# Optimization experiments

Hardware: AMD Instinct MI355X
Metric: run time of the kernel (lower is better)

Reference implementation:

```python
import jax, jax.numpy as jnp
import numpy as np

N, E = 50000, 800000
IN_FEATS, H, F = 128, 2, 64
NEG_SLOPE = 0.2


def _gat_conv(x, W, attn_l, attn_r, bias, src, dst):
    """DGL-style GATConv. x:[N,IN], W:[H*F,IN], attn_l/attn_r:[H,F], bias:[H*F]. Returns [N,H,F]."""
    z = (x @ W.T).reshape(N, H, F)                      # node projections
    el = jnp.einsum('nhf,hf->nh', z, attn_l)            # [N,H]
    er = jnp.einsum('nhf,hf->nh', z, attn_r)            # [N,H]
    e = jax.nn.leaky_relu(el[src] + er[dst], NEG_SLOPE) # [E,H] edge logits
    # edge softmax over incoming edges of each destination node
    m = jax.ops.segment_max(e, dst, num_segments=N)     # [N,H]
    ex = jnp.exp(e - m[dst])
    s = jax.ops.segment_sum(ex, dst, num_segments=N)    # [N,H]
    alpha = ex / s[dst]                                 # [E,H]
    msg = alpha[:, :, None] * z[src]                    # [E,H,F]
    out = jax.ops.segment_sum(msg, dst, num_segments=N) # [N,H,F]
    return out + bias.reshape(1, H, F)


def setup_inputs() -> dict:
    key = jax.random.key(0)
    ks = jax.random.split(key, 10)
    x = jax.random.normal(ks[0], (N, IN_FEATS), dtype=jnp.float32)
    h = jax.random.normal(ks[1], (N, H, F), dtype=jnp.float32)
    src = jax.random.randint(ks[2], (E,), 0, N, dtype=jnp.int32)
    dst = jax.random.randint(ks[3], (E,), 0, N, dtype=jnp.int32)
    sc = 1.0 / np.sqrt(IN_FEATS)
    W = jax.random.normal(ks[4], (3, H * F, IN_FEATS), dtype=jnp.float32) * sc  # r,u,c fc weights
    attn_l = jax.random.normal(ks[5], (3, H, F), dtype=jnp.float32) * 0.1
    attn_r = jax.random.normal(ks[6], (3, H, F), dtype=jnp.float32) * 0.1
    conv_bias = jax.random.normal(ks[7], (3, H * F), dtype=jnp.float32) * 0.02
    gate_bias = jax.random.uniform(ks[8], (3, H, F), dtype=jnp.float32)  # torch.rand init
    return {"x": x, "h": h, "W": W, "attn_l": attn_l, "attn_r": attn_r,
            "conv_bias": conv_bias, "gate_bias": gate_bias, "src": src, "dst": dst}


def reference(x, h, W, attn_l, attn_r, conv_bias, gate_bias, src, dst):
    # r, u, c gates; each GATConv is applied to x (use_hidden=False branch)
    r = jax.nn.sigmoid(_gat_conv(x, W[0], attn_l[0], attn_r[0], conv_bias[0], src, dst) + gate_bias[0])
    u = jax.nn.sigmoid(_gat_conv(x, W[1], attn_l[1], attn_r[1], conv_bias[1], src, dst) + gate_bias[1])
    # note: original computes h_ = r*h but never uses it in this branch (dead code)
    c = jax.nn.sigmoid(_gat_conv(x, W[2], attn_l[2], attn_r[2], conv_bias[2], src, dst) + gate_bias[2])
    new_h = u * h + (1.0 - u) * c
    return new_h
```

## Files before the change

### kernel.cpp

```cpp
#include <hip/hip_runtime.h>
#include <hip/hip_bf16.h>
#include <math.h>

#define NN 50000
#define EE 800000
#define KIN 128
#define HFD 128
#define ZB 256
#define NB 196
#define GB2 1564
#define SB 782
#define CAP 56
#define BSH 7

typedef __bf16 bf16_t;
typedef __bf16 bf16x8 __attribute__((ext_vector_type(8)));
typedef float f32x2 __attribute__((ext_vector_type(2)));
typedef float f32x4 __attribute__((ext_vector_type(4)));
typedef unsigned short u16;
typedef unsigned int u32;
typedef unsigned char u8;

__device__ __forceinline__ float ldf(const void* p, size_t i, int isf32) {
    return isf32 ? ((const float*)p)[i] : (float)((const bf16_t*)p)[i];
}
__device__ __forceinline__ bf16x8 load8bf(const void* base, size_t off, int isf32) {
    if (isf32) {
        const float4* p = (const float4*)((const float*)base + off);
        float4 u = p[0], v = p[1];
        bf16x8 r;
        r[0] = (bf16_t)u.x; r[1] = (bf16_t)u.y; r[2] = (bf16_t)u.z; r[3] = (bf16_t)u.w;
        r[4] = (bf16_t)v.x; r[5] = (bf16_t)v.y; r[6] = (bf16_t)v.z; r[7] = (bf16_t)v.w;
        return r;
    }
    return *(const bf16x8*)((const bf16_t*)base + off);
}

__device__ __forceinline__ uint2 pack8f(const float* v) {
    u32 lo = __builtin_amdgcn_cvt_pk_fp8_f32(v[0], v[1], 0u, false);
    lo = __builtin_amdgcn_cvt_pk_fp8_f32(v[2], v[3], lo, true);
    u32 hi = __builtin_amdgcn_cvt_pk_fp8_f32(v[4], v[5], 0u, false);
    hi = __builtin_amdgcn_cvt_pk_fp8_f32(v[6], v[7], hi, true);
    return make_uint2(lo, hi);
}

__global__ __launch_bounds__(256) void k_front(const unsigned short* __restrict__ xw,
                                               const void* __restrict__ W,
                                               const void* __restrict__ attn_l,
                                               const void* __restrict__ attn_r,
                                               u8* __restrict__ bkt,
                                               int* __restrict__ dflag,
                                               bf16_t* __restrict__ walv)
{
    const int b = blockIdx.x, tid = threadIdx.x;
    int i = b * 256 + tid;
    if (i < NN) *(int*)(bkt + ((size_t)i << BSH)) = 0;
    if (b > 8) return;

    __shared__ int cnt;
    if (tid == 0) cnt = 0;
    __syncthreads();
    int c = 0;
    for (int k = tid; k < 2048; k += 256) {
        int e = (xw[k] >> 7) & 0xFF;
        if (e > 150) c++;
    }
    atomicAdd(&cnt, c);
    __syncthreads();
    const int isf32 = (cnt > 20) ? 1 : 0;

    if (b == 0) {
        if (tid == 0) dflag[0] = isf32;
        return;
    }
    const int c8 = b - 1;
    const int side = c8 >> 2, g = (c8 >> 1) & 1, h = c8 & 1;
    const void* attn = side ? attn_r : attn_l;
    const int k = tid;
    if (k < KIN) {
        float acc = 0.f;
        for (int f = 0; f < 64; f++) {
            float wv = ldf(W, ((size_t)(g + 1) * HFD + h * 64 + f) * KIN + k, isf32);
            float av = ldf(attn, (size_t)((g + 1) * 2 + h) * 64 + f, isf32);
            acc += wv * av;
        }
        walv[(size_t)c8 * KIN + k] = (bf16_t)(acc * 1.44269504f);
    }
}

__global__ __launch_bounds__(256) void k_big(const void* __restrict__ x,
                                             const void* __restrict__ W,
                                             const bf16_t* __restrict__ walv,
                                             u8* __restrict__ z8,
                                             float* __restrict__ eln,
                                             float* __restrict__ ern,
                                             const int* __restrict__ src,
                                             const int* __restrict__ dst,
                                             u8* __restrict__ bkt,
                                             const int* __restrict__ dflag)
{
    __shared__ bf16_t wlds[128 * 128];

    const int bx = blockIdx.x;
    if (bx % 3 == 2) {
        int base = (bx / 3) * 1024 + threadIdx.x * 4;
        if (base < EE) {
            int4 s4 = *(const int4*)(src + base);
            int4 d4 = *(const int4*)(dst + base);
            u8* r0 = bkt + ((size_t)d4.x << BSH);
            u8* r1 = bkt + ((size_t)d4.y << BSH);
            u8* r2 = bkt + ((size_t)d4.z << BSH);
            u8* r3 = bkt + ((size_t)d4.w << BSH);
            int p0 = atomicAdd((int*)r0, 1);
            int p1 = atomicAdd((int*)r1, 1);
            int p2 = atomicAdd((int*)r2, 1);
            int p3 = atomicAdd((int*)r3, 1);
            if (p0 < CAP) *(u16*)(r0 + 4 + 2 * p0) = (u16)s4.x;
            if (p1 < CAP) *(u16*)(r1 + 4 + 2 * p1) = (u16)s4.y;
            if (p2 < CAP) *(u16*)(r2 + 4 + 2 * p2) = (u16)s4.z;
            if (p3 < CAP) *(u16*)(r3 + 4 + 2 * p3) = (u16)s4.w;
        }
        return;
    }

    const int isf32 = dflag[0];
    const int tid = threadIdx.x;
    const int gid = (bx / 3) * 2 + (bx % 3);
    const int ng = gid >> 1;
    const int g  = gid & 1;

    for (int c = tid; c < 2048; c += 256) {
        int col = c >> 4, g8 = c & 15;
        bf16x8 v = load8bf(W, ((size_t)(g + 1) * HFD + col) * KIN + g8 * 8, isf32);
        *(bf16x8*)(wlds + (size_t)col * 128 + (g8 ^ (col & 15)) * 8) = v;
    }

    const int wave = tid >> 6;
    const int lane = tid & 63;
    const int quad = lane >> 4;
    const int lm   = lane & 15;
    const int node_base = ng * 64 + wave * 16;

    int nld = node_base + lm;
    if (nld > NN - 1) nld = NN - 1;

    bf16x8 a[4];
#pragma unroll
    for (int kk = 0; kk < 4; kk++)
        a[kk] = load8bf(x, (size_t)nld * KIN + kk * 32 + quad * 8, isf32);

    __syncthreads();

    f32x4 acc[8];
#pragma unroll
    for (int t = 0; t < 8; t++) {
        const int wc = t * 16 + lm;
        f32x4 a4 = {0.f, 0.f, 0.f, 0.f};
#pragma unroll
        for (int kk = 0; kk < 4; kk++) {
            bf16x8 b = *(const bf16x8*)(wlds + (size_t)wc * 128 + ((kk * 4 + quad) ^ lm) * 8);
            a4 = __builtin_amdgcn_mfma_f32_16x16x32_bf16(a[kk], b, a4, 0, 0, 0);
        }
        acc[t] = a4;
    }

    if (g == 0) {
        f32x4 sacc = {0.f, 0.f, 0.f, 0.f};
#pragma unroll
        for (int kk = 0; kk < 4; kk++) {
            bf16x8 b;
            if (lm < 8) b = *(const bf16x8*)(walv + (size_t)lm * KIN + kk * 32 + quad * 8);
            else {
#pragma unroll
                for (int jj = 0; jj < 8; jj++) b[jj] = (bf16_t)0.f;
            }
            sacc = __builtin_amdgcn_mfma_f32_16x16x32_bf16(a[kk], b, sacc, 0, 0, 0);
        }
#pragma unroll
        for (int r = 0; r < 4; r++) {
            int nn = node_base + quad * 4 + r;
            if (nn < NN) {
                if (lm < 4)      eln[(size_t)nn * 4 + lm] = sacc[r];
                else if (lm < 8) ern[(size_t)nn * 4 + (lm - 4)] = sacc[r];
            }
        }
    }

#pragma unroll
    for (int r = 0; r < 4; r++) {
        float f[8];
#pragma unroll
        for (int t = 0; t < 8; t++) f[t] = acc[t][r];
        uint2 u = pack8f(f);
        int node = node_base + quad * 4 + r;
        if (node < NN)
            *(uint2*)(z8 + (size_t)node * ZB + g * 128 + lm * 8) = u;
    }
}

__global__ __launch_bounds__(256) void k_agg(const u8* __restrict__ z8,
                                             const u8* __restrict__ bkt,
                                             const float* __restrict__ eln,
                                             const float* __restrict__ ern,
                                             const void* __restrict__ conv_bias,
                                             const void* __restrict__ gate_bias,
                                             const void* __restrict__ hin,
                                             void* __restrict__ out,
                                             const int* __restrict__ dflag)
{
    const int isf32 = dflag[0];
    const int wave = threadIdx.x >> 6;
    const int lane = threadIdx.x & 63;
    const int j = ((lane >> 5) << 1) | (lane & 1);
    const int n = blockIdx.x * 4 + wave;
    if (n >= NN) return;
    const u8* rb = bkt + ((size_t)n << BSH);
    int cnt = *(const int*)rb;
    if (cnt > CAP) cnt = CAP;
    const u16* row = (const u16*)(rb + 4);
    const u32* row32 = (const u32*)row;
    const float erj = ern[(size_t)n * 4 + j];
    const u32 zoff = 4u * (u32)lane;

    float a0 = 0.f, a1 = 0.f, a2 = 0.f, a3 = 0.f, s = 0.f;
    int i = 0;
    for (; i + 8 <= cnt; i += 8) {
        u32 rr[4];
#pragma unroll
        for (int q = 0; q < 4; q++) rr[q] = row32[(i >> 1) + q];
        u32 sn[8];
#pragma unroll
        for (int q = 0; q < 4; q++) { sn[2*q] = rr[q] & 0xFFFF; sn[2*q+1] = rr[q] >> 16; }
        u32 zb[8];
#pragma unroll
        for (int q = 0; q < 8; q++)
            zb[q] = *(const u32*)(z8 + ((sn[q] << 8) + zoff));
        float w[8];
#pragma unroll
        for (int q = 0; q < 8; q++) {
            float v = eln[sn[q] * 4 + (u32)j] + erj;
            v = v > 0.f ? v : 0.2f * v;
            w[q] = exp2f(v);
        }
#pragma unroll
        for (int q = 0; q < 8; q++) {
            f32x2 lo = __builtin_amdgcn_cvt_pk_f32_fp8(zb[q], false);
            f32x2 hi = __builtin_amdgcn_cvt_pk_f32_fp8(zb[q], true);
            a0 += w[q] * lo[0];
            a1 += w[q] * lo[1];
            a2 += w[q] * hi[0];
            a3 += w[q] * hi[1];
            s += w[q];
        }
    }
    if (i + 4 <= cnt) {
        u32 rr[2];
#pragma unroll
        for (int q = 0; q < 2; q++) rr[q] = row32[(i >> 1) + q];
        u32 sn[4];
#pragma unroll
        for (int q = 0; q < 2; q++) { sn[2*q] = rr[q] & 0xFFFF; sn[2*q+1] = rr[q] >> 16; }
        u32 zb[4];
#pragma unroll
        for (int q = 0; q < 4; q++)
            zb[q] = *(const u32*)(z8 + ((sn[q] << 8) + zoff));
#pragma unroll
        for (int q = 0; q < 4; q++) {
            float v = eln[sn[q] * 4 + (u32)j] + erj;
            v = v > 0.f ? v : 0.2f * v;
            float w = exp2f(v);
            f32x2 lo = __builtin_amdgcn_cvt_pk_f32_fp8(zb[q], false);
            f32x2 hi = __builtin_amdgcn_cvt_pk_f32_fp8(zb[q], true);
            a0 += w * lo[0];
            a1 += w * lo[1];
            a2 += w * hi[0];
            a3 += w * hi[1];
            s += w;
        }
        i += 4;
    }
    for (; i < cnt; i++) {
        u32 sn = row[i];
        u32 zb = *(const u32*)(z8 + ((sn << 8) + zoff));
        float v = eln[sn * 4 + (u32)j] + erj;
        v = v > 0.f ? v : 0.2f * v;
        float w = exp2f(v);
        f32x2 lo = __builtin_amdgcn_cvt_pk_f32_fp8(zb, false);
        f32x2 hi = __builtin_amdgcn_cvt_pk_f32_fp8(zb, true);
        a0 += w * lo[0];
        a1 += w * lo[1];
        a2 += w * hi[0];
        a3 += w * hi[1];
        s += w;
    }

    float inv = (cnt > 0) ? 1.f / fmaxf(s, 1e-30f) : 0.f;
    float o[4] = {a0 * inv, a1 * inv, a2 * inv, a3 * inv};

    const int gate = lane >> 5;
    int cf[4];
#pragma unroll
    for (int u = 0; u < 4; u++) cf[u] = (4 * (lane & 1) + u) * 16 + ((lane & 31) >> 1);

    float res[4];
    float hh[4];
    if (lane < 32) {
#pragma unroll
        for (int u = 0; u < 4; u++)
            hh[u] = ldf(hin, (size_t)n * HFD + cf[u], isf32);
    }
#pragma unroll
    for (int u = 0; u < 4; u++) {
        float ob = ldf(conv_bias, (size_t)(gate + 1) * HFD + cf[u], isf32)
                 + ldf(gate_bias, (size_t)((gate + 1) * 2 + (lane & 1)) * 64 + (cf[u] & 63), isf32);
        float gv = 1.f / (1.f + __expf(-(o[u] + ob)));
        float other = __shfl(gv, lane ^ 32, 64);
        if (lane < 32)
            res[u] = gv * hh[u] + (1.f - gv) * other;
    }
    if (lane < 32) {
        if (isf32) {
#pragma unroll
            for (int u = 0; u < 4; u++)
                ((float*)out)[(size_t)n * HFD + cf[u]] = res[u];
        } else {
#pragma unroll
            for (int u = 0; u < 4; u++)
                ((bf16_t*)out)[(size_t)n * HFD + cf[u]] = (bf16_t)res[u];
        }
    }
}

extern "C" void kernel_launch(void* const* d_in, const int* in_sizes, int n_in,
                              void* d_out, int out_size, void* d_ws, size_t ws_size,
                              hipStream_t stream)
{
    const void* x         = d_in[0];
    const void* hin       = d_in[1];
    const void* W         = d_in[2];
    const void* attn_l    = d_in[3];
    const void* attn_r    = d_in[4];
    const void* conv_bias = d_in[5];
    const void* gate_bias = d_in[6];
    const int* src        = (const int*)d_in[7];
    const int* dst        = (const int*)d_in[8];

    char* p = (char*)d_ws;
    int* dflag    = (int*)p;    p += 256;
    u8* z8        = (u8*)p;     p += (size_t)NN * ZB;
    float* eln    = (float*)p;  p += (size_t)NN * 4 * 4;
    float* ern    = (float*)p;  p += (size_t)NN * 4 * 4;
    u8* bkt       = (u8*)p;     p += (size_t)NN << BSH;
    bf16_t* walv  = (bf16_t*)p; p += 8 * KIN * 2;

    k_front<<<NB, 256, 0, stream>>>((const unsigned short*)x, W, attn_l, attn_r,
                                    bkt, dflag, walv);
    k_big<<<GB2 + SB, 256, 0, stream>>>(x, W, walv, z8, eln, ern, src, dst,
                                        bkt, dflag);
    k_agg<<<(NN + 3) / 4, 256, 0, stream>>>(z8, bkt, eln, ern,
                                            conv_bias, gate_bias, hin, d_out, dflag);
}
```

Baseline: 220.7 us.

## Move bucket count to row tail and software-pipeline aggregation gathers

Moves the per-node edge counter from the head of each 128-byte bucket row to offset 112, so source indices start 16-byte aligned and can be fetched with four vector loads up front. The aggregation loop is restructured into 8-edge tiles with double-buffered issue/compute, so gathers for the next tile overlap math on the current one. Partial tiles are handled by masking weights to zero, with indices clamped to stay in range. This trades some wasted loads and ALU work on padded edges for more memory-level parallelism and fewer scalar index loads.

```diff
diff --git a/kernel.cpp b/kernel.cpp
--- a/kernel.cpp
+++ b/kernel.cpp
@@ -44,6 +44,39 @@
     return make_uint2(lo, hi);
 }
 
+__device__ __forceinline__ void unpack8(uint4 v, u32 sn[8]) {
+    sn[0] = v.x & 0xFFFFu; sn[1] = v.x >> 16;
+    sn[2] = v.y & 0xFFFFu; sn[3] = v.y >> 16;
+    sn[4] = v.z & 0xFFFFu; sn[5] = v.z >> 16;
+    sn[6] = v.w & 0xFFFFu; sn[7] = v.w >> 16;
+#pragma unroll
+    for (int q = 0; q < 8; q++) sn[q] = sn[q] < NN ? sn[q] : (NN - 1);
+}
+__device__ __forceinline__ void issue8(const u8* __restrict__ z8, const float* __restrict__ eln,
+                                       const u32 sn[8], u32 zoff, u32 j,
+                                       u32 zb[8], float el[8]) {
+#pragma unroll
+    for (int q = 0; q < 8; q++) {
+        zb[q] = *(const u32*)(z8 + (sn[q] << 8) + zoff);
+        el[q] = eln[sn[q] * 4u + j];
+    }
+}
+__device__ __forceinline__ void comp8(const u32 zb[8], const float el[8], float erj, int m,
+                                      float& a0, float& a1, float& a2, float& a3, float& s) {
+#pragma unroll
+    for (int q = 0; q < 8; q++) {
+        float v = el[q] + erj;
+        v = fmaxf(v, 0.2f * v);
+        float w = exp2f(v);
+        if (q >= m) w = 0.f;
+        f32x2 lo = __builtin_amdgcn_cvt_pk_f32_fp8(zb[q], false);
+        f32x2 hi = __builtin_amdgcn_cvt_pk_f32_fp8(zb[q], true);
+        a0 += w * lo[0]; a1 += w * lo[1];
+        a2 += w * hi[0]; a3 += w * hi[1];
+        s += w;
+    }
+}
+
 __global__ __launch_bounds__(256) void k_front(const unsigned short* __restrict__ xw,
                                                const void* __restrict__ W,
                                                const void* __restrict__ attn_l,
@@ -54,7 +87,7 @@
 {
     const int b = blockIdx.x, tid = threadIdx.x;
     int i = b * 256 + tid;
-    if (i < NN) *(int*)(bkt + ((size_t)i << BSH)) = 0;
+    if (i < NN) *(int*)(bkt + ((size_t)i << BSH) + 112) = 0;
     if (b > 8) return;
 
     __shared__ int cnt;
@@ -111,14 +144,14 @@
             u8* r1 = bkt + ((size_t)d4.y << BSH);
             u8* r2 = bkt + ((size_t)d4.z << BSH);
             u8* r3 = bkt + ((size_t)d4.w << BSH);
-            int p0 = atomicAdd((int*)r0, 1);
-            int p1 = atomicAdd((int*)r1, 1);
-            int p2 = atomicAdd((int*)r2, 1);
-            int p3 = atomicAdd((int*)r3, 1);
-            if (p0 < CAP) *(u16*)(r0 + 4 + 2 * p0) = (u16)s4.x;
-            if (p1 < CAP) *(u16*)(r1 + 4 + 2 * p1) = (u16)s4.y;
-            if (p2 < CAP) *(u16*)(r2 + 4 + 2 * p2) = (u16)s4.z;
-            if (p3 < CAP) *(u16*)(r3 + 4 + 2 * p3) = (u16)s4.w;
+            int p0 = atomicAdd((int*)(r0 + 112), 1);
+            int p1 = atomicAdd((int*)(r1 + 112), 1);
+            int p2 = atomicAdd((int*)(r2 + 112), 1);
+            int p3 = atomicAdd((int*)(r3 + 112), 1);
+            if (p0 < CAP) *(u16*)(r0 + 2 * p0) = (u16)s4.x;
+            if (p1 < CAP) *(u16*)(r1 + 2 * p1) = (u16)s4.y;
+            if (p2 < CAP) *(u16*)(r2 + 2 * p2) = (u16)s4.z;
+            if (p3 < CAP) *(u16*)(r3 + 2 * p3) = (u16)s4.w;
         }
         return;
     }
@@ -211,87 +244,50 @@
     const int isf32 = dflag[0];
     const int wave = threadIdx.x >> 6;
     const int lane = threadIdx.x & 63;
-    const int j = ((lane >> 5) << 1) | (lane & 1);
+    const u32 j = ((lane >> 5) << 1) | (lane & 1);
     const int n = blockIdx.x * 4 + wave;
     if (n >= NN) return;
     const u8* rb = bkt + ((size_t)n << BSH);
-    int cnt = *(const int*)rb;
+    int cnt = *(const int*)(rb + 112);
+    uint4 q0 = *(const uint4*)(rb);
+    uint4 q1 = *(const uint4*)(rb + 16);
+    uint4 q2 = *(const uint4*)(rb + 32);
+    uint4 q3 = *(const uint4*)(rb + 48);
     if (cnt > CAP) cnt = CAP;
-    const u16* row = (const u16*)(rb + 4);
-    const u32* row32 = (const u32*)row;
     const float erj = ern[(size_t)n * 4 + j];
     const u32 zoff = 4u * (u32)lane;
 
     float a0 = 0.f, a1 = 0.f, a2 = 0.f, a3 = 0.f, s = 0.f;
-    int i = 0;
-    for (; i + 8 <= cnt; i += 8) {
-        u32 rr[4];
-#pragma unroll
-        for (int q = 0; q < 4; q++) rr[q] = row32[(i >> 1) + q];
-        u32 sn[8];
-#pragma unroll
-        for (int q = 0; q < 4; q++) { sn[2*q] = rr[q] & 0xFFFF; sn[2*q+1] = rr[q] >> 16; }
-        u32 zb[8];
-#pragma unroll
-        for (int q = 0; q < 8; q++)
-            zb[q] = *(const u32*)(z8 + ((sn[q] << 8) + zoff));
-        float w[8];
-#pragma unroll
-        for (int q = 0; q < 8; q++) {
-            float v = eln[sn[q] * 4 + (u32)j] + erj;
-            v = v > 0.f ? v : 0.2f * v;
-            w[q] = exp2f(v);
-        }
-#pragma unroll
-        for (int q = 0; q < 8; q++) {
-            f32x2 lo = __builtin_amdgcn_cvt_pk_f32_fp8(zb[q], false);
-            f32x2 hi = __builtin_amdgcn_cvt_pk_f32_fp8(zb[q], true);
-            a0 += w[q] * lo[0];
-            a1 += w[q] * lo[1];
-            a2 += w[q] * hi[0];
-            a3 += w[q] * hi[1];
-            s += w[q];
-        }
-    }
-    if (i + 4 <= cnt) {
-        u32 rr[2];
-#pragma unroll
-        for (int q = 0; q < 2; q++) rr[q] = row32[(i >> 1) + q];
-        u32 sn[4];
-#pragma unroll
-        for (int q = 0; q < 2; q++) { sn[2*q] = rr[q] & 0xFFFF; sn[2*q+1] = rr[q] >> 16; }
-        u32 zb[4];
-#pragma unroll
-        for (int q = 0; q < 4; q++)
-            zb[q] = *(const u32*)(z8 + ((sn[q] << 8) + zoff));
-#pragma unroll
-        for (int q = 0; q < 4; q++) {
-            float v = eln[sn[q] * 4 + (u32)j] + erj;
-            v = v > 0.f ? v : 0.2f * v;
-            float w = exp2f(v);
-            f32x2 lo = __builtin_amdgcn_cvt_pk_f32_fp8(zb[q], false);
-            f32x2 hi = __builtin_amdgcn_cvt_pk_f32_fp8(zb[q], true);
-            a0 += w * lo[0];
-            a1 += w * lo[1];
-            a2 += w * hi[0];
-            a3 += w * hi[1];
-            s += w;
-        }
-        i += 4;
-    }
-    for (; i < cnt; i++) {
-        u32 sn = row[i];
-        u32 zb = *(const u32*)(z8 + ((sn << 8) + zoff));
-        float v = eln[sn * 4 + (u32)j] + erj;
-        v = v > 0.f ? v : 0.2f * v;
-        float w = exp2f(v);
-        f32x2 lo = __builtin_amdgcn_cvt_pk_f32_fp8(zb, false);
-        f32x2 hi = __builtin_amdgcn_cvt_pk_f32_fp8(zb, true);
-        a0 += w * lo[0];
-        a1 += w * lo[1];
-        a2 += w * hi[0];
-        a3 += w * hi[1];
-        s += w;
+    u32 snA[8], snB[8], zbA[8], zbB[8];
+    float elA[8], elB[8];
+
+    if (cnt <= 32) {
+        const int nt = (cnt + 7) >> 3;
+        if (nt >= 1) { unpack8(q0, snA); issue8(z8, eln, snA, zoff, j, zbA, elA); }
+        if (nt >= 2) { unpack8(q1, snB); issue8(z8, eln, snB, zoff, j, zbB, elB); }
+        if (nt >= 1) comp8(zbA, elA, erj, cnt,      a0, a1, a2, a3, s);
+        if (nt >= 3) { unpack8(q2, snA); issue8(z8, eln, snA, zoff, j, zbA, elA); }
+        if (nt >= 2) comp8(zbB, elB, erj, cnt - 8,  a0, a1, a2, a3, s);
+        if (nt >= 4) { unpack8(q3, snB); issue8(z8, eln, snB, zoff, j, zbB, elB); }
+        if (nt >= 3) comp8(zbA, elA, erj, cnt - 16, a0, a1, a2, a3, s);
+        if (nt >= 4) comp8(zbB, elB, erj, cnt - 24, a0, a1, a2, a3, s);
+    } else {
+        unpack8(q0, snA); issue8(z8, eln, snA, zoff, j, zbA, elA);
+        unpack8(q1, snB); issue8(z8, eln, snB, zoff, j, zbB, elB);
+        comp8(zbA, elA, erj, 8, a0, a1, a2, a3, s);
+        unpack8(q2, snA); issue8(z8, eln, snA, zoff, j, zbA, elA);
+        comp8(zbB, elB, erj, 8, a0, a1, a2, a3, s);
+        unpack8(q3, snB); issue8(z8, eln, snB, zoff, j, zbB, elB);
+        comp8(zbA, elA, erj, 8, a0, a1, a2, a3, s);
+        comp8(zbB, elB, erj, 8, a0, a1, a2, a3, s);
+        const u32* r32 = (const u32*)rb;
+        for (int i = 32; i < cnt; i += 8) {
+            uint4 v;
+            v.x = r32[(i >> 1)];     v.y = r32[(i >> 1) + 1];
+            v.z = r32[(i >> 1) + 2]; v.w = r32[(i >> 1) + 3];
+            unpack8(v, snA); issue8(z8, eln, snA, zoff, j, zbA, elA);
+            comp8(zbA, elA, erj, cnt - i, a0, a1, a2, a3, s);
+        }
     }
 
     float inv = (cnt > 0) ? 1.f / fmaxf(s, 1e-30f) : 0.f;
```

After: 232.9 us. +5.5%, slower.
